# Kernel tuning notes

Hardware: AMD Instinct MI355X
Metric: run time of the kernel (lower is better)

## Reference

```python
import jax, jax.numpy as jnp
import numpy as np
import math

H = 5       # attention heads
DK = 20     # attdim // H
ATT = 100   # attdim
LAYERS = 2
B, L, BERT_DIM = 32, 256, 768


def _layernorm(x, a, b, eps=1e-6):
    mean = x.mean(-1, keepdims=True)
    std = jnp.std(x, axis=-1, ddof=1, keepdims=True)  # torch.std is unbiased
    return a * (x - mean) / (std + eps) + b


def _forward(sequence_output, src_mask, aspect_mask, short_mask,
             ln_a, ln_b, Wxx_w, Wxx_b, q_w, q_b, k_w, k_b,
             dense_w, dense_b, bias_m, W_w, W_b, Wx_w, Wx_b, clf_w, clf_b):
    Bn, Ln, _ = sequence_output.shape
    x = _layernorm(sequence_output, ln_a, ln_b)
    g = x @ Wxx_w + Wxx_b                                  # [B,L,100]
    asp_wn = aspect_mask.sum(1, keepdims=True)             # [B,1]
    aspect = (g * aspect_mask[..., None]).sum(1) / asp_wn  # [B,100]

    q = (g @ q_w + q_b).reshape(Bn, Ln, H, DK).transpose(0, 2, 1, 3)  # [B,H,L,dk]
    k = (g @ k_w + k_b).reshape(Bn, Ln, H, DK).transpose(0, 2, 1, 3)
    # aspect is expanded identically across heads/positions before dense -> [B,dk]
    asp = aspect @ dense_w + dense_b                       # [B,dk]
    scores = jnp.einsum('bhid,bhjd->bhij', q, k) / math.sqrt(DK)
    asp_sc = jnp.tanh(jnp.einsum('bd,bhjd->bhj', asp, k) + bias_m[0])
    scores = scores + asp_sc[:, :, None, :]
    scores = jnp.where(src_mask[:, None, None, :] == 0, -1e9, scores)
    scores = scores + short_mask                           # [B,1,L,L] broadcast
    adj = jax.nn.softmax(scores, axis=-1)                  # [B,H,L,L]

    # edge-update linear split so the [B,L,L,205] concat is never materialized:
    # edge[b,i,j] = adj_perm[b,i,j] @ Wa + go[b,j] @ W1 + go[b,i] @ W2 + b
    Wa, W1, W2 = Wx_w[:H], Wx_w[H:H + ATT], Wx_w[H + ATT:]
    go = g
    for i in range(LAYERS):
        # expand+matmul+mean over heads == mean-head message passing
        Ax = jnp.einsum('bhij,bjd->bid', adj, go) / H
        go = jax.nn.relu(Ax @ W_w + W_b)
        if i < LAYERS - 1:  # last edge update is discarded by the original output
            edge = (jnp.einsum('bhij,hk->bijk', adj, Wa)
                    + (go @ W1)[:, None, :, :]
                    + (go @ W2)[:, :, None, :]
                    + Wx_b)
            adj = edge.transpose(0, 3, 1, 2)
    # original: node_outputs = F.relu(gcn_outputs) (aggregate_W result is overwritten)
    h = jax.nn.relu(go)
    out1 = (h * aspect_mask[..., None]).sum(1) / asp_wn    # [B,100]
    return out1 @ clf_w + clf_b                            # [B,3]


def setup_inputs() -> dict:
    key = jax.random.key(0)
    ks = jax.random.split(key, 24)
    f32 = jnp.float32
    p = lambda k, shape, s=0.05: jax.random.normal(k, shape, dtype=f32) * s
    src_mask = jax.random.randint(ks[0], (B, L), 0, 2, dtype=jnp.int32).at[:, 0].set(1)
    aspect_mask = jnp.zeros((B, L), f32).at[:, 4:8].set(1.0)  # aspect span tokens
    return {
        'sequence_output': jax.random.normal(ks[1], (B, L, BERT_DIM), dtype=f32),
        'src_mask': src_mask,
        'aspect_mask': aspect_mask,
        'short_mask': p(ks[2], (B, 1, L, L), 1.0),
        'ln_a': jnp.ones((BERT_DIM,), f32),
        'ln_b': jnp.zeros((BERT_DIM,), f32),
        'Wxx_w': p(ks[3], (BERT_DIM, ATT)), 'Wxx_b': p(ks[4], (ATT,)),
        'q_w': p(ks[5], (ATT, ATT)), 'q_b': p(ks[6], (ATT,)),
        'k_w': p(ks[7], (ATT, ATT)), 'k_b': p(ks[8], (ATT,)),
        'dense_w': p(ks[9], (ATT, DK)), 'dense_b': p(ks[10], (DK,)),
        'bias_m': p(ks[11], (1,)),
        'W_w': p(ks[12], (ATT, ATT)), 'W_b': p(ks[13], (ATT,)),
        'Wx_w': p(ks[14], (H + 2 * ATT, H)), 'Wx_b': p(ks[15], (H,)),
        'clf_w': p(ks[16], (ATT, 3)), 'clf_b': p(ks[17], (3,)),
    }


def reference(sequence_output, src_mask, aspect_mask, short_mask,
              ln_a, ln_b, Wxx_w, Wxx_b, q_w, q_b, k_w, k_b,
              dense_w, dense_b, bias_m, W_w, W_b, Wx_w, Wx_b, clf_w, clf_b):
    return _forward(sequence_output, src_mask, aspect_mask, short_mask,
                    ln_a, ln_b, Wxx_w, Wxx_b, q_w, q_b, k_w, k_b,
                    dense_w, dense_b, bias_m, W_w, W_b, Wx_w, Wx_b, clf_w, clf_b)
```

## Files before the change

### kernel.cpp

```cpp
#include <hip/hip_runtime.h>
#include <math.h>

constexpr int CL = 256;
constexpr int CD = 768;
constexpr int CATT = 100;
constexpr int CH = 5;
constexpr int CDK = 20;

__device__ __forceinline__ void fma4(float4& a, float s, const float4& w) {
    a.x = fmaf(s, w.x, a.x);
    a.y = fmaf(s, w.y, a.y);
    a.z = fmaf(s, w.z, a.z);
    a.w = fmaf(s, w.w, a.w);
}

__device__ __forceinline__ void gl2lds16(const void* gsrc, void* ldst) {
    __builtin_amdgcn_global_load_lds(
        (const __attribute__((address_space(1))) void*)gsrc,
        (__attribute__((address_space(3))) void*)ldst, 16, 0, 0);
}

__global__ __launch_bounds__(256, 3) void k1_fused(
    const float* __restrict__ x, const float* __restrict__ ln_a,
    const float* __restrict__ ln_b, const float* __restrict__ Wxx_w,
    const float* __restrict__ Wxx_b, const float* __restrict__ q_w,
    const float* __restrict__ q_b, const float* __restrict__ k_w,
    const float* __restrict__ k_b, const float* __restrict__ amask,
    float* __restrict__ g, float* __restrict__ qt, float* __restrict__ ktb,
    float* __restrict__ aspect_raw)
{
    __shared__ float s_w[2][3200];
    __shared__ float s_xn[2][16 * 36];
    __shared__ float s_gt[16 * 100];
    __shared__ float s_ln[1536];
// ... 150 lines not shown
                float4 rv[2] = { p0, p1 };
#pragma unroll
                for (int q = 0; q < 2; ++q) {
                    int row = r0 + rg * 2 + q;
                    int bidx = row >> 8, l = row & 255;
                    *(float4*)&outp[((size_t)(bidx * CH + h) * CL + l) * CDK + d] = rv[q];
                }
                p0 = make_float4(0.f, 0.f, 0.f, 0.f);
                p1 = make_float4(0.f, 0.f, 0.f, 0.f);
            }
        }
        __syncthreads();
    }
}

__global__ __launch_bounds__(256, 3) void k45_attn_gcn0(
    const float* __restrict__ qt, const float* __restrict__ ktb,
    const float* __restrict__ aspect_raw, const float* __restrict__ amask,
    const float* __restrict__ dense_w, const float* __restrict__ dense_b,
    const float* __restrict__ bias_m, const int* __restrict__ src_mask,
    const float* __restrict__ shortm, const float* __restrict__ Wx_w,
    const float* __restrict__ g, const float* __restrict__ W_w,
    const float* __restrict__ W_b, float* __restrict__ adjW,
    float* __restrict__ go1, float* __restrict__ t1, float* __restrict__ t2,
    float* __restrict__ gW2S)
{
    constexpr int ICH = 16;
    __shared__ float s_pool[16 * 260];
    __shared__ float s_w[2][3200];
    __shared__ float s_q[CH * 320];
    __shared__ float s_red[CH][64];
    __shared__ float s_was[5];
    __shared__ float s_aspb[20];
    __shared__ float s_w1[100], s_w2[100];
    __shared__ float s_g1row[16];

    const int b = blockIdx.x >> 4, ic = blockIdx.x & 15;
    const int i0 = ic * ICH;
    const int t = threadIdx.x, lane = t & 63, wid = t >> 6;
    const int j = t;

    if (t < 5) {
        float s = 0.f;
        for (int k2 = 0; k2 < 5; ++k2) s += Wx_w[t * 5 + k2];
        s_was[t] = s;
    }
    if (t < 100) {
        float a = 0.f, c2 = 0.f;
#pragma unroll
        for (int h = 0; h < 5; ++h) {
            a += Wx_w[(5 + t) * 5 + h];
            c2 += Wx_w[(105 + t) * 5 + h];
        }
        s_w1[t] = a; s_w2[t] = c2;
    }
    float wn = 0.f;
    if (t < 64) {
        float4 mv = ((const float4*)amask)[b * 64 + t];
        wn = mv.x + mv.y + mv.z + mv.w;
#pragma unroll
        for (int o = 32; o; o >>= 1) wn += __shfl_xor(wn, o);
    }
    if (t < 20) {
        float a = 0.f;
        for (int d = 0; d < CATT; ++d)
            a = fmaf(aspect_raw[b * CATT + d], dense_w[d * CDK + t], a);
        s_aspb[t] = a / wn + dense_b[t];
    }
    {
        const float* qbase = qt + (size_t)b * CH * CL * CDK + (size_t)i0 * CDK;
        for (int i = t; i < CH * 320; i += 256) {
            int h = i / 320, r = i % 320;
            s_q[i] = qbase[(size_t)h * CL * CDK + r];
        }
    }

    const bool masked = (src_mask[b * CL + j] == 0);
    const float bm = bias_m[0];
    const float rs20 = 0.223606797749978969f;

    float sm[ICH];
#pragma unroll
    for (int ii = 0; ii < ICH; ++ii)
        sm[ii] = shortm[(size_t)(b * CL + i0 + ii) * CL + j];

    float accS[ICH], accW[ICH];
#pragma unroll
    for (int ii = 0; ii < ICH; ++ii) { accS[ii] = 0.f; accW[ii] = 0.f; }

    __syncthreads();

    for (int h = 0; h < CH; ++h) {
        float4 kr[5];
        const float* kp = ktb + ((size_t)(b * CH + h) * CL + j) * CDK;
#pragma unroll
        for (int m = 0; m < 5; ++m) kr[m] = *(const float4*)(kp + 4 * m);
        const float was_h = s_was[h];
        float s = bm;
#pragma unroll
        for (int m = 0; m < 5; ++m) {
            s = fmaf(s_aspb[4 * m + 0], kr[m].x, s);
            s = fmaf(s_aspb[4 * m + 1], kr[m].y, s);
            s = fmaf(s_aspb[4 * m + 2], kr[m].z, s);
            s = fmaf(s_aspb[4 * m + 3], kr[m].w, s);
        }
        const float aspsc = tanhf(s);

        float pv[ICH];
#pragma unroll
        for (int ii = 0; ii < ICH; ++ii) {
            const float* qrow = &s_q[h * 320 + ii * CDK];
            float sc = 0.f;
#pragma unroll
            for (int m = 0; m < 5; ++m) {
                float4 q4 = *(const float4*)(qrow + 4 * m);
                sc = fmaf(q4.x, kr[m].x, sc);
                sc = fmaf(q4.y, kr[m].y, sc);
                sc = fmaf(q4.z, kr[m].z, sc);
                sc = fmaf(q4.w, kr[m].w, sc);
            }
            sc = fmaf(sc, rs20, aspsc) + sm[ii];
            float p = masked ? 0.f : __expf(sc);
            pv[ii] = p;
            float ssum = p;
#pragma unroll
            for (int o = 32; o; o >>= 1) ssum += __shfl_xor(ssum, o);
            if (lane == 0) s_red[h][ii * 4 + wid] = ssum;
        }
        __syncthreads();
#pragma unroll
        for (int ii = 0; ii < ICH; ++ii) {
            float tot = s_red[h][ii * 4 + 0] + s_red[h][ii * 4 + 1] +
                        s_red[h][ii * 4 + 2] + s_red[h][ii * 4 + 3];
            float pn = pv[ii] * __frcp_rn(tot);
            accS[ii] += pn;
            accW[ii] = fmaf(was_h, pn, accW[ii]);
        }
    }

#pragma unroll
    for (int ii = 0; ii < ICH; ++ii) {
        adjW[(size_t)(b * CL + i0 + ii) * CL + j] = accW[ii];
        s_pool[ii * 260 + j] = accS[ii];
    }

    const int cg = t % 25, rg = t / 25;
    const int c = cg * 4;
    const float4* g4 = (const float4*)g + (size_t)b * 6400;
    gl2lds16(g4 + t,       &s_w[0][(t      ) * 4]);
    gl2lds16(g4 + t + 256, &s_w[0][(t + 256) * 4]);
    gl2lds16(g4 + t + 512, &s_w[0][(t + 512) * 4]);
    if (t < 32) gl2lds16(g4 + t + 768, &s_w[0][(t + 768) * 4]);
    __syncthreads();

    float4 acc0 = make_float4(0.f, 0.f, 0.f, 0.f);
    float4 acc1 = make_float4(0.f, 0.f, 0.f, 0.f);
    for (int jt = 0; jt < 8; ++jt) {
        if (jt < 7) {
            const float4* src = g4 + (size_t)(jt + 1) * 800;
            float* wd = s_w[(jt + 1) & 1];
            gl2lds16(src + t,       wd + (t      ) * 4);
            gl2lds16(src + t + 256, wd + (t + 256) * 4);
            gl2lds16(src + t + 512, wd + (t + 512) * 4);
            if (t < 32) gl2lds16(src + t + 768, wd + (t + 768) * 4);
        }
        if (t < 200) {
            const float* wb = s_w[jt & 1];
#pragma unroll 2
            for (int kk = 0; kk < 32; kk += 4) {
                float4 a0 = *(const float4*)&s_pool[(rg * 2 + 0) * 260 + jt * 32 + kk];
                float4 a1 = *(const float4*)&s_pool[(rg * 2 + 1) * 260 + jt * 32 + kk];
                float4 v0 = *(const float4*)&wb[(kk + 0) * 100 + c];
                float4 v1 = *(const float4*)&wb[(kk + 1) * 100 + c];
                float4 v2 = *(const float4*)&wb[(kk + 2) * 100 + c];
                float4 v3 = *(const float4*)&wb[(kk + 3) * 100 + c];
                fma4(acc0, a0.x, v0); fma4(acc0, a0.y, v1); fma4(acc0, a0.z, v2); fma4(acc0, a0.w, v3);
                fma4(acc1, a1.x, v0); fma4(acc1, a1.y, v1); fma4(acc1, a1.z, v2); fma4(acc1, a1.w, v3);
            }
        }
        __syncthreads();
    }

    float* s_ax = s_pool;
    if (t < 200) {
        float4 r;
        r.x = acc0.x * 0.2f; r.y = acc0.y * 0.2f; r.z = acc0.z * 0.2f; r.w = acc0.w * 0.2f;
        *(float4*)&s_ax[(rg * 2 + 0) * 108 + c] = r;
        r.x = acc1.x * 0.2f; r.y = acc1.y * 0.2f; r.z = acc1.z * 0.2f; r.w = acc1.w * 0.2f;
        *(float4*)&s_ax[(rg * 2 + 1) * 108 + c] = r;
    }
    const float4* ww4 = (const float4*)W_w;
    gl2lds16(ww4 + t, &s_w[0][t * 4]);
    if (t < 244) gl2lds16(ww4 + t + 256, &s_w[0][(t + 256) * 4]);
    __syncthreads();

    float4 o0 = make_float4(0.f, 0.f, 0.f, 0.f);
    float4 o1 = make_float4(0.f, 0.f, 0.f, 0.f);
    for (int wt = 0; wt < 5; ++wt) {
        if (wt < 4) {
            const float4* src = ww4 + (size_t)(wt + 1) * 500;
            float* wd = s_w[(wt + 1) & 1];
            gl2lds16(src + t, wd + t * 4);
            if (t < 244) gl2lds16(src + t + 256, wd + (t + 256) * 4);
        }
        if (t < 200) {
            const float* wb = s_w[wt & 1];
            const int kb = wt * 20;
#pragma unroll 2
            for (int kk = 0; kk < 20; kk += 4) {
                float4 a0 = *(const float4*)&s_ax[(rg * 2 + 0) * 108 + kb + kk];
                float4 a1 = *(const float4*)&s_ax[(rg * 2 + 1) * 108 + kb + kk];
                float4 v0 = *(const float4*)&wb[(kk + 0) * 100 + c];
                float4 v1 = *(const float4*)&wb[(kk + 1) * 100 + c];
                float4 v2 = *(const float4*)&wb[(kk + 2) * 100 + c];
                float4 v3 = *(const float4*)&wb[(kk + 3) * 100 + c];
                fma4(o0, a0.x, v0); fma4(o0, a0.y, v1); fma4(o0, a0.z, v2); fma4(o0, a0.w, v3);
                fma4(o1, a1.x, v0); fma4(o1, a1.y, v1); fma4(o1, a1.z, v2); fma4(o1, a1.w, v3);
            }
        }
        __syncthreads();
    }

    float* s_go = s_pool + 1728;
    if (t < 200) {
        float4 bias = *(const float4*)&W_b[c];
        o0.x = fmaxf(o0.x + bias.x, 0.f); o0.y = fmaxf(o0.y + bias.y, 0.f);
        o0.z = fmaxf(o0.z + bias.z, 0.f); o0.w = fmaxf(o0.w + bias.w, 0.f);
        o1.x = fmaxf(o1.x + bias.x, 0.f); o1.y = fmaxf(o1.y + bias.y, 0.f);
        o1.z = fmaxf(o1.z + bias.z, 0.f); o1.w = fmaxf(o1.w + bias.w, 0.f);
        *(float4*)&go1[(size_t)(b * CL + i0 + rg * 2 + 0) * CATT + c] = o0;
        *(float4*)&go1[(size_t)(b * CL + i0 + rg * 2 + 1) * CATT + c] = o1;
        *(float4*)&s_go[(rg * 2 + 0) * 104 + c] = o0;
        *(float4*)&s_go[(rg * 2 + 1) * 104 + c] = o1;
    }
    __syncthreads();

    if (t < 128) {
        int r = t >> 3, seg = t & 7;
        int e0 = seg * 13, e1 = e0 + 13 < 100 ? e0 + 13 : 100;
        float a = 0.f, c2 = 0.f;
        for (int e = e0; e < e1; ++e) {
            float v = s_go[r * 104 + e];
            a = fmaf(v, s_w1[e], a);
            c2 = fmaf(v, s_w2[e], c2);
        }
        a += __shfl_xor(a, 1); a += __shfl_xor(a, 2); a += __shfl_xor(a, 4);
        c2 += __shfl_xor(c2, 1); c2 += __shfl_xor(c2, 2); c2 += __shfl_xor(c2, 4);
        if (seg == 0) {
            s_g1row[r] = a;
            gW2S[b * CL + i0 + r] = c2;
        }
    }
    __syncthreads();

    if (t < 100) {
        float a = 0.f, s2 = 0.f;
#pragma unroll
        for (int r = 0; r < 16; ++r) {
            float v = s_go[r * 104 + t];
            a = fmaf(s_g1row[r], v, a);
            s2 += v;
        }
        atomicAdd(&t1[b * CATT + t], a);
        atomicAdd(&t2[b * CATT + t], s2);
    }
}

__global__ __launch_bounds__(256, 3) void k7_gcn1(
    const float* __restrict__ adjW, const float* __restrict__ go1,
    const float* __restrict__ W_w, const float* __restrict__ W_b,
    const float* __restrict__ t1, const float* __restrict__ t2,
    const float* __restrict__ gW2S, const float* __restrict__ Wx_b,
    const float* __restrict__ amask, float* __restrict__ out1_raw)
{
    __shared__ float s_pool[16 * 260];
    __shared__ float s_w[2][3200];
    const int b = blockIdx.x >> 4, ic = blockIdx.x & 15;
    const int i0 = ic * 16;
    const int t = threadIdx.x;

    {
        const float4* asrc = (const float4*)adjW + (size_t)(b * CL + i0) * 64;
#pragma unroll
        for (int m = 0; m < 4; ++m) {
            int i = t + 256 * m;
            gl2lds16(asrc + i, &s_pool[(i >> 6) * 260 + (i & 63) * 4]);
        }
    }
    const int cg = t % 25, rg = t / 25;
    const int c = cg * 4;
    const float4* g4 = (const float4*)go1 + (size_t)b * 6400;
    gl2lds16(g4 + t,       &s_w[0][(t      ) * 4]);
    gl2lds16(g4 + t + 256, &s_w[0][(t + 256) * 4]);
    gl2lds16(g4 + t + 512, &s_w[0][(t + 512) * 4]);
    if (t < 32) gl2lds16(g4 + t + 768, &s_w[0][(t + 768) * 4]);
    __syncthreads();

    float4 acc0 = make_float4(0.f, 0.f, 0.f, 0.f);
    float4 acc1 = make_float4(0.f, 0.f, 0.f, 0.f);
    for (int jt = 0; jt < 8; ++jt) {
        if (jt < 7) {
            const float4* src = g4 + (size_t)(jt + 1) * 800;
            float* wd = s_w[(jt + 1) & 1];
            gl2lds16(src + t,       wd + (t      ) * 4);
            gl2lds16(src + t + 256, wd + (t + 256) * 4);
            gl2lds16(src + t + 512, wd + (t + 512) * 4);
            if (t < 32) gl2lds16(src + t + 768, wd + (t + 768) * 4);
        }
        if (t < 200) {
            const float* wb = s_w[jt & 1];
#pragma unroll 2
            for (int kk = 0; kk < 32; kk += 4) {
                float4 a0 = *(const float4*)&s_pool[(rg * 2 + 0) * 260 + jt * 32 + kk];
                float4 a1 = *(const float4*)&s_pool[(rg * 2 + 1) * 260 + jt * 32 + kk];
                float4 v0 = *(const float4*)&wb[(kk + 0) * 100 + c];
                float4 v1 = *(const float4*)&wb[(kk + 1) * 100 + c];
                float4 v2 = *(const float4*)&wb[(kk + 2) * 100 + c];
                float4 v3 = *(const float4*)&wb[(kk + 3) * 100 + c];
                fma4(acc0, a0.x, v0); fma4(acc0, a0.y, v1); fma4(acc0, a0.z, v2); fma4(acc0, a0.w, v3);
                fma4(acc1, a1.x, v0); fma4(acc1, a1.y, v1); fma4(acc1, a1.z, v2); fma4(acc1, a1.w, v3);
            }
        }
        __syncthreads();
    }

    float* s_ax = s_pool;
    if (t < 200) {
        float wxbs = Wx_b[0] + Wx_b[1] + Wx_b[2] + Wx_b[3] + Wx_b[4];
        float4 t1v = *(const float4*)&t1[b * CATT + c];
        float4 t2v = *(const float4*)&t2[b * CATT + c];
        float gw0 = gW2S[b * CL + i0 + rg * 2 + 0] + wxbs;
        float gw1 = gW2S[b * CL + i0 + rg * 2 + 1] + wxbs;
        float4 r;
        r.x = (acc0.x + t1v.x + gw0 * t2v.x) * 0.2f;
        r.y = (acc0.y + t1v.y + gw0 * t2v.y) * 0.2f;
        r.z = (acc0.z + t1v.z + gw0 * t2v.z) * 0.2f;
        r.w = (acc0.w + t1v.w + gw0 * t2v.w) * 0.2f;
        *(float4*)&s_ax[(rg * 2 + 0) * 108 + c] = r;
        r.x = (acc1.x + t1v.x + gw1 * t2v.x) * 0.2f;
        r.y = (acc1.y + t1v.y + gw1 * t2v.y) * 0.2f;
        r.z = (acc1.z + t1v.z + gw1 * t2v.z) * 0.2f;
        r.w = (acc1.w + t1v.w + gw1 * t2v.w) * 0.2f;
        *(float4*)&s_ax[(rg * 2 + 1) * 108 + c] = r;
    }
    const float4* ww4 = (const float4*)W_w;
    gl2lds16(ww4 + t, &s_w[0][t * 4]);
    if (t < 244) gl2lds16(ww4 + t + 256, &s_w[0][(t + 256) * 4]);
    __syncthreads();

    float4 o0 = make_float4(0.f, 0.f, 0.f, 0.f);
    float4 o1 = make_float4(0.f, 0.f, 0.f, 0.f);
    for (int wt = 0; wt < 5; ++wt) {
        if (wt < 4) {
            const float4* src = ww4 + (size_t)(wt + 1) * 500;
            float* wd = s_w[(wt + 1) & 1];
            gl2lds16(src + t, wd + t * 4);
            if (t < 244) gl2lds16(src + t + 256, wd + (t + 256) * 4);
        }
        if (t < 200) {
            const float* wb = s_w[wt & 1];
            const int kb = wt * 20;
#pragma unroll 2
            for (int kk = 0; kk < 20; kk += 4) {
                float4 a0 = *(const float4*)&s_ax[(rg * 2 + 0) * 108 + kb + kk];
                float4 a1 = *(const float4*)&s_ax[(rg * 2 + 1) * 108 + kb + kk];
                float4 v0 = *(const float4*)&wb[(kk + 0) * 100 + c];
                float4 v1 = *(const float4*)&wb[(kk + 1) * 100 + c];
                float4 v2 = *(const float4*)&wb[(kk + 2) * 100 + c];
                float4 v3 = *(const float4*)&wb[(kk + 3) * 100 + c];
                fma4(o0, a0.x, v0); fma4(o0, a0.y, v1); fma4(o0, a0.z, v2); fma4(o0, a0.w, v3);
                fma4(o1, a1.x, v0); fma4(o1, a1.y, v1); fma4(o1, a1.z, v2); fma4(o1, a1.w, v3);
            }
        }
        __syncthreads();
    }

    if (t < 200) {
        float4 bias = *(const float4*)&W_b[c];
        o0.x = fmaxf(o0.x + bias.x, 0.f); o0.y = fmaxf(o0.y + bias.y, 0.f);
        o0.z = fmaxf(o0.z + bias.z, 0.f); o0.w = fmaxf(o0.w + bias.w, 0.f);
        o1.x = fmaxf(o1.x + bias.x, 0.f); o1.y = fmaxf(o1.y + bias.y, 0.f);
        o1.z = fmaxf(o1.z + bias.z, 0.f); o1.w = fmaxf(o1.w + bias.w, 0.f);
        float4 ov[2] = { o0, o1 };
#pragma unroll
        for (int q = 0; q < 2; ++q) {
            int row = b * CL + i0 + rg * 2 + q;
            float m = amask[row];
            if (m != 0.f) {
                atomicAdd(&out1_raw[b * CATT + c + 0], m * ov[q].x);
                atomicAdd(&out1_raw[b * CATT + c + 1], m * ov[q].y);
                atomicAdd(&out1_raw[b * CATT + c + 2], m * ov[q].z);
                atomicAdd(&out1_raw[b * CATT + c + 3], m * ov[q].w);
            }
        }
    }
}

__global__ __launch_bounds__(64) void k8_small(
    const float* __restrict__ out1_raw, const float* __restrict__ amask,
    const float* __restrict__ clf_w, const float* __restrict__ clf_b,
    float* __restrict__ out)
{
    const int b = blockIdx.x, t = threadIdx.x;
    float4 mv = ((const float4*)amask)[b * 64 + t];
    float wn = mv.x + mv.y + mv.z + mv.w;
#pragma unroll
    for (int o = 32; o; o >>= 1) wn += __shfl_xor(wn, o);
    if (t < 3) {
        float rwn = 1.f / wn;
        float a = clf_b[t];
        for (int d = 0; d < CATT; ++d)
            a = fmaf(out1_raw[b * CATT + d] * rwn, clf_w[d * 3 + t], a);
        out[b * 3 + t] = a;
    }
}

extern "C" void kernel_launch(void* const* d_in, const int* in_sizes, int n_in,
                              void* d_out, int out_size, void* d_ws, size_t ws_size,
                              hipStream_t stream) {
    const float* seq     = (const float*)d_in[0];
    const int*   srcm    = (const int*)d_in[1];
    const float* amask   = (const float*)d_in[2];
    const float* shortm  = (const float*)d_in[3];
    const float* ln_a    = (const float*)d_in[4];
    const float* ln_b    = (const float*)d_in[5];
    const float* Wxx_w   = (const float*)d_in[6];
    const float* Wxx_b   = (const float*)d_in[7];
    const float* q_w     = (const float*)d_in[8];
// ... 4 lines not shown
    const float* dense_b = (const float*)d_in[13];
    const float* bias_m  = (const float*)d_in[14];
    const float* W_w     = (const float*)d_in[15];
    const float* W_b     = (const float*)d_in[16];
    const float* Wx_w    = (const float*)d_in[17];
    const float* Wx_b    = (const float*)d_in[18];
    const float* clf_w   = (const float*)d_in[19];
    const float* clf_b   = (const float*)d_in[20];
    float* out = (float*)d_out;

    float* ws         = (float*)d_ws;
    float* g          = ws;
    float* qt         = g + 819200;
    float* ktb        = qt + 819200;
    float* go1        = ktb + 819200;
    float* adjW       = go1 + 819200;
    float* aspect_raw = adjW + 2097152;
    float* t1         = aspect_raw + 3200;
    float* t2         = t1 + 3200;
    float* out1_raw   = t2 + 3200;
    float* gW2S       = out1_raw + 3200;

    hipMemsetAsync(aspect_raw, 0, 4 * 3200 * sizeof(float), stream);
    hipLaunchKernelGGL(k1_fused, dim3(512), dim3(256), 0, stream, seq, ln_a, ln_b,
                       Wxx_w, Wxx_b, q_w, q_b, k_w, k_b, amask, g, qt, ktb, aspect_raw);
    hipLaunchKernelGGL(k45_attn_gcn0, dim3(512), dim3(256), 0, stream,
                       qt, ktb, aspect_raw, amask, dense_w, dense_b, bias_m, srcm,
                       shortm, Wx_w, g, W_w, W_b, adjW, go1, t1, t2, gW2S);
    hipLaunchKernelGGL(k7_gcn1, dim3(512), dim3(256), 0, stream,
                       adjW, go1, W_w, W_b, t1, t2, gW2S, Wx_b, amask, out1_raw);
    hipLaunchKernelGGL(k8_small, dim3(32), dim3(64), 0, stream,
                       out1_raw, amask, clf_w, clf_b, out);
}
```

Baseline: 241.3 us.

## Fuse attention, both GCN layers and classifier into one kernel with per-batch barriers

Merges the attention/GCN0 kernel, the GCN1 kernel and the classifier kernel into one launch. Blocks that share a batch synchronise through per-batch atomic counters in global memory, and the block grid is remapped so that a batch's blocks land on the same XCD. The adjW matrix stays in registers instead of being written to and re-read from global memory, which removes two launches and a large intermediate. The cost is spin-wait barriers that depend on all 16 blocks of a batch being co-resident, which risks deadlock or stalls if occupancy is insufficient.

```diff
diff --git a/kernel.cpp b/kernel.cpp
--- a/kernel.cpp
+++ b/kernel.cpp
@@ -18,6 +18,20 @@
     __builtin_amdgcn_global_load_lds(
         (const __attribute__((address_space(1))) void*)gsrc,
         (__attribute__((address_space(3))) void*)ldst, 16, 0, 0);
+}
+
+__device__ __forceinline__ void bbar(unsigned* ctr, unsigned target, bool poll) {
+    __syncthreads();
+    if (threadIdx.x == 0) {
+        __hip_atomic_fetch_add(ctr, 1u, __ATOMIC_RELEASE, __HIP_MEMORY_SCOPE_AGENT);
+        if (poll) {
+            while (__hip_atomic_load(ctr, __ATOMIC_RELAXED, __HIP_MEMORY_SCOPE_AGENT) < target) {
+                __builtin_amdgcn_s_sleep(2);
+            }
+        }
+    }
+    __syncthreads();
+    __builtin_amdgcn_fence(__ATOMIC_ACQUIRE, "agent");
 }
 
 __global__ __launch_bounds__(256, 3) void k1_fused(
@@ -198,16 +212,18 @@
     }
 }
 
-__global__ __launch_bounds__(256, 3) void k45_attn_gcn0(
+__global__ __launch_bounds__(256, 3) void k457_fused(
     const float* __restrict__ qt, const float* __restrict__ ktb,
     const float* __restrict__ aspect_raw, const float* __restrict__ amask,
     const float* __restrict__ dense_w, const float* __restrict__ dense_b,
     const float* __restrict__ bias_m, const int* __restrict__ src_mask,
     const float* __restrict__ shortm, const float* __restrict__ Wx_w,
     const float* __restrict__ g, const float* __restrict__ W_w,
-    const float* __restrict__ W_b, float* __restrict__ adjW,
+    const float* __restrict__ W_b, const float* __restrict__ Wx_b,
+    const float* __restrict__ clf_w, const float* __restrict__ clf_b,
     float* __restrict__ go1, float* __restrict__ t1, float* __restrict__ t2,
-    float* __restrict__ gW2S)
+    float* __restrict__ out1_raw, unsigned* __restrict__ bar,
+    float* __restrict__ out)
 {
     constexpr int ICH = 16;
     __shared__ float s_pool[16 * 260];
@@ -218,384 +234,375 @@
     __shared__ float s_aspb[20];
     __shared__ float s_w1[100], s_w2[100];
     __shared__ float s_g1row[16];
-
-    const int b = blockIdx.x >> 4, ic = blockIdx.x & 15;
+    __shared__ float s_gw2[16];
+
+    const int t = threadIdx.x, lane = t & 63, wid = t >> 6;
+    const int xcd = blockIdx.x & 7;
+    const int slot = blockIdx.x >> 3;
+    const int b = xcd * 4 + (slot >> 4);
+    const int ic = slot & 15;
     const int i0 = ic * ICH;
-    const int t = threadIdx.x, lane = t & 63, wid = t >> 6;
     const int j = t;
-
-    if (t < 5) {
-        float s = 0.f;
-        for (int k2 = 0; k2 < 5; ++k2) s += Wx_w[t * 5 + k2];
-        s_was[t] = s;
-    }
-    if (t < 100) {
-        float a = 0.f, c2 = 0.f;
-#pragma unroll
-        for (int h = 0; h < 5; ++h) {
-            a += Wx_w[(5 + t) * 5 + h];
-            c2 += Wx_w[(105 + t) * 5 + h];
-        }
-        s_w1[t] = a; s_w2[t] = c2;
-    }
-    float wn = 0.f;
-    if (t < 64) {
-        float4 mv = ((const float4*)amask)[b * 64 + t];
-        wn = mv.x + mv.y + mv.z + mv.w;
-#pragma unroll
-        for (int o = 32; o; o >>= 1) wn += __shfl_xor(wn, o);
-    }
-    if (t < 20) {
-        float a = 0.f;
-        for (int d = 0; d < CATT; ++d)
-            a = fmaf(aspect_raw[b * CATT + d], dense_w[d * CDK + t], a);
-        s_aspb[t] = a / wn + dense_b[t];
-    }
+    unsigned* bctr = bar + b * 32;
+
+    float accW[ICH];
     {
-        const float* qbase = qt + (size_t)b * CH * CL * CDK + (size_t)i0 * CDK;
-        for (int i = t; i < CH * 320; i += 256) {
-            int h = i / 320, r = i % 320;
-            s_q[i] = qbase[(size_t)h * CL * CDK + r];
-        }
-    }
-
-    const bool masked = (src_mask[b * CL + j] == 0);
-    const float bm = bias_m[0];
-    const float rs20 = 0.223606797749978969f;
-
-    float sm[ICH];
-#pragma unroll
-    for (int ii = 0; ii < ICH; ++ii)
-        sm[ii] = shortm[(size_t)(b * CL + i0 + ii) * CL + j];
-
-    float accS[ICH], accW[ICH];
-#pragma unroll
-    for (int ii = 0; ii < ICH; ++ii) { accS[ii] = 0.f; accW[ii] = 0.f; }
-
-    __syncthreads();
-
-    for (int h = 0; h < CH; ++h) {
-        float4 kr[5];
-        const float* kp = ktb + ((size_t)(b * CH + h) * CL + j) * CDK;
-#pragma unroll
-        for (int m = 0; m < 5; ++m) kr[m] = *(const float4*)(kp + 4 * m);
-        const float was_h = s_was[h];
-        float s = bm;
-#pragma unroll
-        for (int m = 0; m < 5; ++m) {
-            s = fmaf(s_aspb[4 * m + 0], kr[m].x, s);
-            s = fmaf(s_aspb[4 * m + 1], kr[m].y, s);
-            s = fmaf(s_aspb[4 * m + 2], kr[m].z, s);
-            s = fmaf(s_aspb[4 * m + 3], kr[m].w, s);
-        }
-        const float aspsc = tanhf(s);
-
-        float pv[ICH];
-#pragma unroll
-        for (int ii = 0; ii < ICH; ++ii) {
-            const float* qrow = &s_q[h * 320 + ii * CDK];
-            float sc = 0.f;
+        if (t < 5) {
+            float s = 0.f;
+            for (int k2 = 0; k2 < 5; ++k2) s += Wx_w[t * 5 + k2];
+            s_was[t] = s;
+        }
+        if (t < 100) {
+            float a = 0.f, c2 = 0.f;
+#pragma unroll
+            for (int h = 0; h < 5; ++h) {
+                a += Wx_w[(5 + t) * 5 + h];
+                c2 += Wx_w[(105 + t) * 5 + h];
+            }
+            s_w1[t] = a; s_w2[t] = c2;
+        }
+        float wn = 0.f;
+        if (t < 64) {
+            float4 mv = ((const float4*)amask)[b * 64 + t];
+            wn = mv.x + mv.y + mv.z + mv.w;
+#pragma unroll
+            for (int o = 32; o; o >>= 1) wn += __shfl_xor(wn, o);
+        }
+        if (t < 20) {
+            float a = 0.f;
+            for (int d = 0; d < CATT; ++d)
+                a = fmaf(aspect_raw[b * CATT + d], dense_w[d * CDK + t], a);
+            s_aspb[t] = a / wn + dense_b[t];
+        }
+        {
+            const float* qbase = qt + (size_t)b * CH * CL * CDK + (size_t)i0 * CDK;
+            for (int i = t; i < CH * 320; i += 256) {
+                int h = i / 320, r = i % 320;
+                s_q[i] = qbase[(size_t)h * CL * CDK + r];
+            }
+        }
+
+        const bool masked = (src_mask[b * CL + j] == 0);
+        const float bm = bias_m[0];
+        const float rs20 = 0.223606797749978969f;
+
+        float sm[ICH];
+#pragma unroll
+        for (int ii = 0; ii < ICH; ++ii)
+            sm[ii] = shortm[(size_t)(b * CL + i0 + ii) * CL + j];
+
+        float accS[ICH];
+#pragma unroll
+        for (int ii = 0; ii < ICH; ++ii) { accS[ii] = 0.f; accW[ii] = 0.f; }
+
+        __syncthreads();
+
+        for (int h = 0; h < CH; ++h) {
+            float4 kr[5];
+            const float* kp = ktb + ((size_t)(b * CH + h) * CL + j) * CDK;
+#pragma unroll
+            for (int m = 0; m < 5; ++m) kr[m] = *(const float4*)(kp + 4 * m);
+            const float was_h = s_was[h];
+            float s = bm;
 #pragma unroll
             for (int m = 0; m < 5; ++m) {
-                float4 q4 = *(const float4*)(qrow + 4 * m);
-                sc = fmaf(q4.x, kr[m].x, sc);
-                sc = fmaf(q4.y, kr[m].y, sc);
-                sc = fmaf(q4.z, kr[m].z, sc);
-                sc = fmaf(q4.w, kr[m].w, sc);
-            }
-            sc = fmaf(sc, rs20, aspsc) + sm[ii];
-            float p = masked ? 0.f : __expf(sc);
-            pv[ii] = p;
-            float ssum = p;
-#pragma unroll
-            for (int o = 32; o; o >>= 1) ssum += __shfl_xor(ssum, o);
-            if (lane == 0) s_red[h][ii * 4 + wid] = ssum;
-        }
-        __syncthreads();
-#pragma unroll
-        for (int ii = 0; ii < ICH; ++ii) {
-            float tot = s_red[h][ii * 4 + 0] + s_red[h][ii * 4 + 1] +
-                        s_red[h][ii * 4 + 2] + s_red[h][ii * 4 + 3];
-            float pn = pv[ii] * __frcp_rn(tot);
-            accS[ii] += pn;
-            accW[ii] = fmaf(was_h, pn, accW[ii]);
-        }
-    }
-
-#pragma unroll
-    for (int ii = 0; ii < ICH; ++ii) {
-        adjW[(size_t)(b * CL + i0 + ii) * CL + j] = accW[ii];
-        s_pool[ii * 260 + j] = accS[ii];
+                s = fmaf(s_aspb[4 * m + 0], kr[m].x, s);
+                s = fmaf(s_aspb[4 * m + 1], kr[m].y, s);
+                s = fmaf(s_aspb[4 * m + 2], kr[m].z, s);
+                s = fmaf(s_aspb[4 * m + 3], kr[m].w, s);
+            }
+            const float aspsc = tanhf(s);
+
+            float pv[ICH];
+#pragma unroll
+            for (int ii = 0; ii < ICH; ++ii) {
+                const float* qrow = &s_q[h * 320 + ii * CDK];
+                float sc = 0.f;
+#pragma unroll
+                for (int m = 0; m < 5; ++m) {
+                    float4 q4 = *(const float4*)(qrow + 4 * m);
+                    sc = fmaf(q4.x, kr[m].x, sc);
+                    sc = fmaf(q4.y, kr[m].y, sc);
+                    sc = fmaf(q4.z, kr[m].z, sc);
+                    sc = fmaf(q4.w, kr[m].w, sc);
+                }
+                sc = fmaf(sc, rs20, aspsc) + sm[ii];
+                float p = masked ? 0.f : __expf(sc);
+                pv[ii] = p;
+                float ssum = p;
+#pragma unroll
+                for (int o = 32; o; o >>= 1) ssum += __shfl_xor(ssum, o);
+                if (lane == 0) s_red[h][ii * 4 + wid] = ssum;
+            }
+            __syncthreads();
+#pragma unroll
+            for (int ii = 0; ii < ICH; ++ii) {
+                float tot = s_red[h][ii * 4 + 0] + s_red[h][ii * 4 + 1] +
+                            s_red[h][ii * 4 + 2] + s_red[h][ii * 4 + 3];
+                float pn = pv[ii] * __frcp_rn(tot);
+                accS[ii] += pn;
+                accW[ii] = fmaf(was_h, pn, accW[ii]);
+            }
+        }
+
+#pragma unroll
+        for (int ii = 0; ii < ICH; ++ii)
+            s_pool[ii * 260 + j] = accS[ii];
     }
 
     const int cg = t % 25, rg = t / 25;
     const int c = cg * 4;
-    const float4* g4 = (const float4*)g + (size_t)b * 6400;
-    gl2lds16(g4 + t,       &s_w[0][(t      ) * 4]);
-    gl2lds16(g4 + t + 256, &s_w[0][(t + 256) * 4]);
-    gl2lds16(g4 + t + 512, &s_w[0][(t + 512) * 4]);
-    if (t < 32) gl2lds16(g4 + t + 768, &s_w[0][(t + 768) * 4]);
-    __syncthreads();
-
-    float4 acc0 = make_float4(0.f, 0.f, 0.f, 0.f);
-    float4 acc1 = make_float4(0.f, 0.f, 0.f, 0.f);
-    for (int jt = 0; jt < 8; ++jt) {
-        if (jt < 7) {
-            const float4* src = g4 + (size_t)(jt + 1) * 800;
-            float* wd = s_w[(jt + 1) & 1];
-            gl2lds16(src + t,       wd + (t      ) * 4);
-            gl2lds16(src + t + 256, wd + (t + 256) * 4);
-            gl2lds16(src + t + 512, wd + (t + 512) * 4);
-            if (t < 32) gl2lds16(src + t + 768, wd + (t + 768) * 4);
-        }
+
+    {
+        const float4* g4 = (const float4*)g + (size_t)b * 6400;
+        gl2lds16(g4 + t,       &s_w[0][(t      ) * 4]);
+        gl2lds16(g4 + t + 256, &s_w[0][(t + 256) * 4]);
+        gl2lds16(g4 + t + 512, &s_w[0][(t + 512) * 4]);
+        if (t < 32) gl2lds16(g4 + t + 768, &s_w[0][(t + 768) * 4]);
+        __syncthreads();
+
+        float4 acc0 = make_float4(0.f, 0.f, 0.f, 0.f);
+        float4 acc1 = make_float4(0.f, 0.f, 0.f, 0.f);
+        for (int jt = 0; jt < 8; ++jt) {
+            if (jt < 7) {
+                const float4* src = g4 + (size_t)(jt + 1) * 800;
+                float* wd = s_w[(jt + 1) & 1];
+                gl2lds16(src + t,       wd + (t      ) * 4);
+                gl2lds16(src + t + 256, wd + (t + 256) * 4);
+                gl2lds16(src + t + 512, wd + (t + 512) * 4);
+                if (t < 32) gl2lds16(src + t + 768, wd + (t + 768) * 4);
+            }
+            if (t < 200) {
+                const float* wb = s_w[jt & 1];
+#pragma unroll 2
+                for (int kk = 0; kk < 32; kk += 4) {
+                    float4 a0 = *(const float4*)&s_pool[(rg * 2 + 0) * 260 + jt * 32 + kk];
+                    float4 a1 = *(const float4*)&s_pool[(rg * 2 + 1) * 260 + jt * 32 + kk];
+                    float4 v0 = *(const float4*)&wb[(kk + 0) * 100 + c];
+                    float4 v1 = *(const float4*)&wb[(kk + 1) * 100 + c];
+                    float4 v2 = *(const float4*)&wb[(kk + 2) * 100 + c];
+                    float4 v3 = *(const float4*)&wb[(kk + 3) * 100 + c];
+                    fma4(acc0, a0.x, v0); fma4(acc0, a0.y, v1); fma4(acc0, a0.z, v2); fma4(acc0, a0.w, v3);
+                    fma4(acc1, a1.x, v0); fma4(acc1, a1.y, v1); fma4(acc1, a1.z, v2); fma4(acc1, a1.w, v3);
+                }
+            }
+            __syncthreads();
+        }
+
+        float* s_ax = s_pool;
         if (t < 200) {
-            const float* wb = s_w[jt & 1];
+            float4 r;
+            r.x = acc0.x * 0.2f; r.y = acc0.y * 0.2f; r.z = acc0.z * 0.2f; r.w = acc0.w * 0.2f;
+            *(float4*)&s_ax[(rg * 2 + 0) * 108 + c] = r;
+            r.x = acc1.x * 0.2f; r.y = acc1.y * 0.2f; r.z = acc1.z * 0.2f; r.w = acc1.w * 0.2f;
+            *(float4*)&s_ax[(rg * 2 + 1) * 108 + c] = r;
+        }
+        const float4* ww4 = (const float4*)W_w;
+        gl2lds16(ww4 + t, &s_w[0][t * 4]);
+        if (t < 244) gl2lds16(ww4 + t + 256, &s_w[0][(t + 256) * 4]);
+        __syncthreads();
+
+        float4 o0 = make_float4(0.f, 0.f, 0.f, 0.f);
+        float4 o1 = make_float4(0.f, 0.f, 0.f, 0.f);
+        for (int wt = 0; wt < 5; ++wt) {
+            if (wt < 4) {
+                const float4* src = ww4 + (size_t)(wt + 1) * 500;
+                float* wd = s_w[(wt + 1) & 1];
+                gl2lds16(src + t, wd + t * 4);
+                if (t < 244) gl2lds16(src + t + 256, wd + (t + 256) * 4);
+            }
+            if (t < 200) {
+                const float* wb = s_w[wt & 1];
+                const int kb = wt * 20;
 #pragma unroll 2
-            for (int kk = 0; kk < 32; kk += 4) {
-                float4 a0 = *(const float4*)&s_pool[(rg * 2 + 0) * 260 + jt * 32 + kk];
-                float4 a1 = *(const float4*)&s_pool[(rg * 2 + 1) * 260 + jt * 32 + kk];
-                float4 v0 = *(const float4*)&wb[(kk + 0) * 100 + c];
-                float4 v1 = *(const float4*)&wb[(kk + 1) * 100 + c];
-                float4 v2 = *(const float4*)&wb[(kk + 2) * 100 + c];
-                float4 v3 = *(const float4*)&wb[(kk + 3) * 100 + c];
-                fma4(acc0, a0.x, v0); fma4(acc0, a0.y, v1); fma4(acc0, a0.z, v2); fma4(acc0, a0.w, v3);
-                fma4(acc1, a1.x, v0); fma4(acc1, a1.y, v1); fma4(acc1, a1.z, v2); fma4(acc1, a1.w, v3);
-            }
-        }
-        __syncthreads();
-    }
-
-    float* s_ax = s_pool;
-    if (t < 200) {
-        float4 r;
-        r.x = acc0.x * 0.2f; r.y = acc0.y * 0.2f; r.z = acc0.z * 0.2f; r.w = acc0.w * 0.2f;
-        *(float4*)&s_ax[(rg * 2 + 0) * 108 + c] = r;
-        r.x = acc1.x * 0.2f; r.y = acc1.y * 0.2f; r.z = acc1.z * 0.2f; r.w = acc1.w * 0.2f;
-        *(float4*)&s_ax[(rg * 2 + 1) * 108 + c] = r;
-    }
-    const float4* ww4 = (const float4*)W_w;
-    gl2lds16(ww4 + t, &s_w[0][t * 4]);
-    if (t < 244) gl2lds16(ww4 + t + 256, &s_w[0][(t + 256) * 4]);
-    __syncthreads();
-
-    float4 o0 = make_float4(0.f, 0.f, 0.f, 0.f);
-    float4 o1 = make_float4(0.f, 0.f, 0.f, 0.f);
-    for (int wt = 0; wt < 5; ++wt) {
-        if (wt < 4) {
-            const float4* src = ww4 + (size_t)(wt + 1) * 500;
-            float* wd = s_w[(wt + 1) & 1];
-            gl2lds16(src + t, wd + t * 4);
-            if (t < 244) gl2lds16(src + t + 256, wd + (t + 256) * 4);
-        }
+                for (int kk = 0; kk < 20; kk += 4) {
+                    float4 a0 = *(const float4*)&s_ax[(rg * 2 + 0) * 108 + kb + kk];
+                    float4 a1 = *(const float4*)&s_ax[(rg * 2 + 1) * 108 + kb + kk];
+                    float4 v0 = *(const float4*)&wb[(kk + 0) * 100 + c];
+                    float4 v1 = *(const float4*)&wb[(kk + 1) * 100 + c];
+                    float4 v2 = *(const float4*)&wb[(kk + 2) * 100 + c];
+                    float4 v3 = *(const float4*)&wb[(kk + 3) * 100 + c];
+                    fma4(o0, a0.x, v0); fma4(o0, a0.y, v1); fma4(o0, a0.z, v2); fma4(o0, a0.w, v3);
+                    fma4(o1, a1.x, v0); fma4(o1, a1.y, v1); fma4(o1, a1.z, v2); fma4(o1, a1.w, v3);
+                }
+            }
+            __syncthreads();
+        }
+
+        float* s_go = s_pool + 1728;
         if (t < 200) {
-            const float* wb = s_w[wt & 1];
-            const int kb = wt * 20;
+            float4 bias = *(const float4*)&W_b[c];
+            o0.x = fmaxf(o0.x + bias.x, 0.f); o0.y = fmaxf(o0.y + bias.y, 0.f);
+            o0.z = fmaxf(o0.z + bias.z, 0.f); o0.w = fmaxf(o0.w + bias.w, 0.f);
+            o1.x = fmaxf(o1.x + bias.x, 0.f); o1.y = fmaxf(o1.y + bias.y, 0.f);
+            o1.z = fmaxf(o1.z + bias.z, 0.f); o1.w = fmaxf(o1.w + bias.w, 0.f);
+            *(float4*)&go1[(size_t)(b * CL + i0 + rg * 2 + 0) * CATT + c] = o0;
+            *(float4*)&go1[(size_t)(b * CL + i0 + rg * 2 + 1) * CATT + c] = o1;
+            *(float4*)&s_go[(rg * 2 + 0) * 104 + c] = o0;
+            *(float4*)&s_go[(rg * 2 + 1) * 104 + c] = o1;
+        }
+        __syncthreads();
+
+        if (t < 128) {
+            int r = t >> 3, seg = t & 7;
+            int e0 = seg * 13, e1 = e0 + 13 < 100 ? e0 + 13 : 100;
+            float a = 0.f, c2 = 0.f;
+            for (int e = e0; e < e1; ++e) {
+                float v = s_go[r * 104 + e];
+                a = fmaf(v, s_w1[e], a);
+                c2 = fmaf(v, s_w2[e], c2);
+            }
+            a += __shfl_xor(a, 1); a += __shfl_xor(a, 2); a += __shfl_xor(a, 4);
+            c2 += __shfl_xor(c2, 1); c2 += __shfl_xor(c2, 2); c2 += __shfl_xor(c2, 4);
+            if (seg == 0) {
+                s_g1row[r] = a;
+                s_gw2[r] = c2;
+            }
+        }
+        __syncthreads();
+
+        if (t < 100) {
+            float a = 0.f, s2 = 0.f;
+#pragma unroll
+            for (int r = 0; r < 16; ++r) {
+                float v = s_go[r * 104 + t];
+                a = fmaf(s_g1row[r], v, a);
+                s2 += v;
+            }
+            atomicAdd(&t1[b * CATT + t], a);
+            atomicAdd(&t2[b * CATT + t], s2);
+        }
+        __syncthreads();
+
+#pragma unroll
+        for (int ii = 0; ii < ICH; ++ii)
+            s_pool[ii * 260 + j] = accW[ii];
+    }
+
+    bbar(bctr, 16, true);
+
+    {
+        const float4* g4 = (const float4*)go1 + (size_t)b * 6400;
+        gl2lds16(g4 + t,       &s_w[0][(t      ) * 4]);
+        gl2lds16(g4 + t + 256, &s_w[0][(t + 256) * 4]);
+        gl2lds16(g4 + t + 512, &s_w[0][(t + 512) * 4]);
+        if (t < 32) gl2lds16(g4 + t + 768, &s_w[0][(t + 768) * 4]);
+        __syncthreads();
+
+        float4 acc0 = make_float4(0.f, 0.f, 0.f, 0.f);
+        float4 acc1 = make_float4(0.f, 0.f, 0.f, 0.f);
+        for (int jt = 0; jt < 8; ++jt) {
+            if (jt < 7) {
+                const float4* src = g4 + (size_t)(jt + 1) * 800;
+                float* wd = s_w[(jt + 1) & 1];
+                gl2lds16(src + t,       wd + (t      ) * 4);
+                gl2lds16(src + t + 256, wd + (t + 256) * 4);
+                gl2lds16(src + t + 512, wd + (t + 512) * 4);
+                if (t < 32) gl2lds16(src + t + 768, wd + (t + 768) * 4);
+            }
+            if (t < 200) {
+                const float* wb = s_w[jt & 1];
 #pragma unroll 2
-            for (int kk = 0; kk < 20; kk += 4) {
-                float4 a0 = *(const float4*)&s_ax[(rg * 2 + 0) * 108 + kb + kk];
-                float4 a1 = *(const float4*)&s_ax[(rg * 2 + 1) * 108 + kb + kk];
-                float4 v0 = *(const float4*)&wb[(kk + 0) * 100 + c];
-                float4 v1 = *(const float4*)&wb[(kk + 1) * 100 + c];
-                float4 v2 = *(const float4*)&wb[(kk + 2) * 100 + c];
-                float4 v3 = *(const float4*)&wb[(kk + 3) * 100 + c];
-                fma4(o0, a0.x, v0); fma4(o0, a0.y, v1); fma4(o0, a0.z, v2); fma4(o0, a0.w, v3);
-                fma4(o1, a1.x, v0); fma4(o1, a1.y, v1); fma4(o1, a1.z, v2); fma4(o1, a1.w, v3);
-            }
-        }
-        __syncthreads();
-    }
-
-    float* s_go = s_pool + 1728;
-    if (t < 200) {
-        float4 bias = *(const float4*)&W_b[c];
-        o0.x = fmaxf(o0.x + bias.x, 0.f); o0.y = fmaxf(o0.y + bias.y, 0.f);
-        o0.z = fmaxf(o0.z + bias.z, 0.f); o0.w = fmaxf(o0.w + bias.w, 0.f);
-        o1.x = fmaxf(o1.x + bias.x, 0.f); o1.y = fmaxf(o1.y + bias.y, 0.f);
-        o1.z = fmaxf(o1.z + bias.z, 0.f); o1.w = fmaxf(o1.w + bias.w, 0.f);
-        *(float4*)&go1[(size_t)(b * CL + i0 + rg * 2 + 0) * CATT + c] = o0;
-        *(float4*)&go1[(size_t)(b * CL + i0 + rg * 2 + 1) * CATT + c] = o1;
-        *(float4*)&s_go[(rg * 2 + 0) * 104 + c] = o0;
-        *(float4*)&s_go[(rg * 2 + 1) * 104 + c] = o1;
-    }
-    __syncthreads();
-
-    if (t < 128) {
-        int r = t >> 3, seg = t & 7;
-        int e0 = seg * 13, e1 = e0 + 13 < 100 ? e0 + 13 : 100;
-        float a = 0.f, c2 = 0.f;
-        for (int e = e0; e < e1; ++e) {
-            float v = s_go[r * 104 + e];
-            a = fmaf(v, s_w1[e], a);
-            c2 = fmaf(v, s_w2[e], c2);
-        }
-        a += __shfl_xor(a, 1); a += __shfl_xor(a, 2); a += __shfl_xor(a, 4);
-        c2 += __shfl_xor(c2, 1); c2 += __shfl_xor(c2, 2); c2 += __shfl_xor(c2, 4);
-        if (seg == 0) {
-            s_g1row[r] = a;
-            gW2S[b * CL + i0 + r] = c2;
-        }
-    }
-    __syncthreads();
-
-    if (t < 100) {
-        float a = 0.f, s2 = 0.f;
-#pragma unroll
-        for (int r = 0; r < 16; ++r) {
-            float v = s_go[r * 104 + t];
-            a = fmaf(s_g1row[r], v, a);
-            s2 += v;
-        }
-        atomicAdd(&t1[b * CATT + t], a);
-        atomicAdd(&t2[b * CATT + t], s2);
-    }
-}
-
-__global__ __launch_bounds__(256, 3) void k7_gcn1(
-    const float* __restrict__ adjW, const float* __restrict__ go1,
-    const float* __restrict__ W_w, const float* __restrict__ W_b,
-    const float* __restrict__ t1, const float* __restrict__ t2,
-    const float* __restrict__ gW2S, const float* __restrict__ Wx_b,
-    const float* __restrict__ amask, float* __restrict__ out1_raw)
-{
-    __shared__ float s_pool[16 * 260];
-    __shared__ float s_w[2][3200];
-    const int b = blockIdx.x >> 4, ic = blockIdx.x & 15;
-    const int i0 = ic * 16;
-    const int t = threadIdx.x;
-
-    {
-        const float4* asrc = (const float4*)adjW + (size_t)(b * CL + i0) * 64;
-#pragma unroll
-        for (int m = 0; m < 4; ++m) {
-            int i = t + 256 * m;
-            gl2lds16(asrc + i, &s_pool[(i >> 6) * 260 + (i & 63) * 4]);
-        }
-    }
-    const int cg = t % 25, rg = t / 25;
-    const int c = cg * 4;
-    const float4* g4 = (const float4*)go1 + (size_t)b * 6400;
-    gl2lds16(g4 + t,       &s_w[0][(t      ) * 4]);
-    gl2lds16(g4 + t + 256, &s_w[0][(t + 256) * 4]);
-    gl2lds16(g4 + t + 512, &s_w[0][(t + 512) * 4]);
-    if (t < 32) gl2lds16(g4 + t + 768, &s_w[0][(t + 768) * 4]);
-    __syncthreads();
-
-    float4 acc0 = make_float4(0.f, 0.f, 0.f, 0.f);
-    float4 acc1 = make_float4(0.f, 0.f, 0.f, 0.f);
-    for (int jt = 0; jt < 8; ++jt) {
-        if (jt < 7) {
-            const float4* src = g4 + (size_t)(jt + 1) * 800;
-            float* wd = s_w[(jt + 1) & 1];
-            gl2lds16(src + t,       wd + (t      ) * 4);
-            gl2lds16(src + t + 256, wd + (t + 256) * 4);
-            gl2lds16(src + t + 512, wd + (t + 512) * 4);
-            if (t < 32) gl2lds16(src + t + 768, wd + (t + 768) * 4);
-        }
+                for (int kk = 0; kk < 32; kk += 4) {
+                    float4 a0 = *(const float4*)&s_pool[(rg * 2 + 0) * 260 + jt * 32 + kk];
+                    float4 a1 = *(const float4*)&s_pool[(rg * 2 + 1) * 260 + jt * 32 + kk];
+                    float4 v0 = *(const float4*)&wb[(kk + 0) * 100 + c];
+                    float4 v1 = *(const float4*)&wb[(kk + 1) * 100 + c];
+                    float4 v2 = *(const float4*)&wb[(kk + 2) * 100 + c];
+                    float4 v3 = *(const float4*)&wb[(kk + 3) * 100 + c];
+                    fma4(acc0, a0.x, v0); fma4(acc0, a0.y, v1); fma4(acc0, a0.z, v2); fma4(acc0, a0.w, v3);
+                    fma4(acc1, a1.x, v0); fma4(acc1, a1.y, v1); fma4(acc1, a1.z, v2); fma4(acc1, a1.w, v3);
+                }
+            }
+            __syncthreads();
+        }
+
+        float* s_ax = s_pool;
         if (t < 200) {
-            const float* wb = s_w[jt & 1];
+            float wxbs = Wx_b[0] + Wx_b[1] + Wx_b[2] + Wx_b[3] + Wx_b[4];
+            float4 t1v = *(const float4*)&t1[b * CATT + c];
+            float4 t2v = *(const float4*)&t2[b * CATT + c];
+            float gw0 = s_gw2[rg * 2 + 0] + wxbs;
+            float gw1 = s_gw2[rg * 2 + 1] + wxbs;
+            float4 r;
+            r.x = (acc0.x + t1v.x + gw0 * t2v.x) * 0.2f;
+            r.y = (acc0.y + t1v.y + gw0 * t2v.y) * 0.2f;
+            r.z = (acc0.z + t1v.z + gw0 * t2v.z) * 0.2f;
+            r.w = (acc0.w + t1v.w + gw0 * t2v.w) * 0.2f;
+            *(float4*)&s_ax[(rg * 2 + 0) * 108 + c] = r;
+            r.x = (acc1.x + t1v.x + gw1 * t2v.x) * 0.2f;
+            r.y = (acc1.y + t1v.y + gw1 * t2v.y) * 0.2f;
+            r.z = (acc1.z + t1v.z + gw1 * t2v.z) * 0.2f;
+            r.w = (acc1.w + t1v.w + gw1 * t2v.w) * 0.2f;
+            *(float4*)&s_ax[(rg * 2 + 1) * 108 + c] = r;
+        }
+        const float4* ww4 = (const float4*)W_w;
+        gl2lds16(ww4 + t, &s_w[0][t * 4]);
+        if (t < 244) gl2lds16(ww4 + t + 256, &s_w[0][(t + 256) * 4]);
+        __syncthreads();
+
+        float4 o0 = make_float4(0.f, 0.f, 0.f, 0.f);
+        float4 o1 = make_float4(0.f, 0.f, 0.f, 0.f);
+        for (int wt = 0; wt < 5; ++wt) {
+            if (wt < 4) {
+                const float4* src = ww4 + (size_t)(wt + 1) * 500;
+                float* wd = s_w[(wt + 1) & 1];
+                gl2lds16(src + t, wd + t * 4);
+                if (t < 244) gl2lds16(src + t + 256, wd + (t + 256) * 4);
+            }
+            if (t < 200) {
+                const float* wb = s_w[wt & 1];
+                const int kb = wt * 20;
 #pragma unroll 2
-            for (int kk = 0; kk < 32; kk += 4) {
-                float4 a0 = *(const float4*)&s_pool[(rg * 2 + 0) * 260 + jt * 32 + kk];
-                float4 a1 = *(const float4*)&s_pool[(rg * 2 + 1) * 260 + jt * 32 + kk];
-                float4 v0 = *(const float4*)&wb[(kk + 0) * 100 + c];
-                float4 v1 = *(const float4*)&wb[(kk + 1) * 100 + c];
-                float4 v2 = *(const float4*)&wb[(kk + 2) * 100 + c];
-                float4 v3 = *(const float4*)&wb[(kk + 3) * 100 + c];
-                fma4(acc0, a0.x, v0); fma4(acc0, a0.y, v1); fma4(acc0, a0.z, v2); fma4(acc0, a0.w, v3);
-                fma4(acc1, a1.x, v0); fma4(acc1, a1.y, v1); fma4(acc1, a1.z, v2); fma4(acc1, a1.w, v3);
-            }
-        }
-        __syncthreads();
-    }
-
-    float* s_ax = s_pool;
-    if (t < 200) {
-        float wxbs = Wx_b[0] + Wx_b[1] + Wx_b[2] + Wx_b[3] + Wx_b[4];
-        float4 t1v = *(const float4*)&t1[b * CATT + c];
-        float4 t2v = *(const float4*)&t2[b * CATT + c];
-        float gw0 = gW2S[b * CL + i0 + rg * 2 + 0] + wxbs;
-        float gw1 = gW2S[b * CL + i0 + rg * 2 + 1] + wxbs;
-        float4 r;
-        r.x = (acc0.x + t1v.x + gw0 * t2v.x) * 0.2f;
-        r.y = (acc0.y + t1v.y + gw0 * t2v.y) * 0.2f;
-        r.z = (acc0.z + t1v.z + gw0 * t2v.z) * 0.2f;
-        r.w = (acc0.w + t1v.w + gw0 * t2v.w) * 0.2f;
-        *(float4*)&s_ax[(rg * 2 + 0) * 108 + c] = r;
-        r.x = (acc1.x + t1v.x + gw1 * t2v.x) * 0.2f;
-        r.y = (acc1.y + t1v.y + gw1 * t2v.y) * 0.2f;
-        r.z = (acc1.z + t1v.z + gw1 * t2v.z) * 0.2f;
-        r.w = (acc1.w + t1v.w + gw1 * t2v.w) * 0.2f;
-        *(float4*)&s_ax[(rg * 2 + 1) * 108 + c] = r;
-    }
-    const float4* ww4 = (const float4*)W_w;
-    gl2lds16(ww4 + t, &s_w[0][t * 4]);
-    if (t < 244) gl2lds16(ww4 + t + 256, &s_w[0][(t + 256) * 4]);
-    __syncthreads();
-
-    float4 o0 = make_float4(0.f, 0.f, 0.f, 0.f);
-    float4 o1 = make_float4(0.f, 0.f, 0.f, 0.f);
-    for (int wt = 0; wt < 5; ++wt) {
-        if (wt < 4) {
-            const float4* src = ww4 + (size_t)(wt + 1) * 500;
-            float* wd = s_w[(wt + 1) & 1];
-            gl2lds16(src + t, wd + t * 4);
-            if (t < 244) gl2lds16(src + t + 256, wd + (t + 256) * 4);
-        }
+                for (int kk = 0; kk < 20; kk += 4) {
+                    float4 a0 = *(const float4*)&s_ax[(rg * 2 + 0) * 108 + kb + kk];
+                    float4 a1 = *(const float4*)&s_ax[(rg * 2 + 1) * 108 + kb + kk];
+                    float4 v0 = *(const float4*)&wb[(kk + 0) * 100 + c];
+                    float4 v1 = *(const float4*)&wb[(kk + 1) * 100 + c];
+                    float4 v2 = *(const float4*)&wb[(kk + 2) * 100 + c];
+                    float4 v3 = *(const float4*)&wb[(kk + 3) * 100 + c];
+                    fma4(o0, a0.x, v0); fma4(o0, a0.y, v1); fma4(o0, a0.z, v2); fma4(o0, a0.w, v3);
+                    fma4(o1, a1.x, v0); fma4(o1, a1.y, v1); fma4(o1, a1.z, v2); fma4(o1, a1.w, v3);
+                }
+            }
+            __syncthreads();
+        }
+
         if (t < 200) {
-            const float* wb = s_w[wt & 1];
-            const int kb = wt * 20;
-#pragma unroll 2
-            for (int kk = 0; kk < 20; kk += 4) {
-                float4 a0 = *(const float4*)&s_ax[(rg * 2 + 0) * 108 + kb + kk];
-                float4 a1 = *(const float4*)&s_ax[(rg * 2 + 1) * 108 + kb + kk];
-                float4 v0 = *(const float4*)&wb[(kk + 0) * 100 + c];
-                float4 v1 = *(const float4*)&wb[(kk + 1) * 100 + c];
-                float4 v2 = *(const float4*)&wb[(kk + 2) * 100 + c];
-                float4 v3 = *(const float4*)&wb[(kk + 3) * 100 + c];
-                fma4(o0, a0.x, v0); fma4(o0, a0.y, v1); fma4(o0, a0.z, v2); fma4(o0, a0.w, v3);
-                fma4(o1, a1.x, v0); fma4(o1, a1.y, v1); fma4(o1, a1.z, v2); fma4(o1, a1.w, v3);
-            }
-        }
-        __syncthreads();
-    }
-
-    if (t < 200) {
-        float4 bias = *(const float4*)&W_b[c];
-        o0.x = fmaxf(o0.x + bias.x, 0.f); o0.y = fmaxf(o0.y + bias.y, 0.f);
-        o0.z = fmaxf(o0.z + bias.z, 0.f); o0.w = fmaxf(o0.w + bias.w, 0.f);
-        o1.x = fmaxf(o1.x + bias.x, 0.f); o1.y = fmaxf(o1.y + bias.y, 0.f);
-        o1.z = fmaxf(o1.z + bias.z, 0.f); o1.w = fmaxf(o1.w + bias.w, 0.f);
-        float4 ov[2] = { o0, o1 };
-#pragma unroll
-        for (int q = 0; q < 2; ++q) {
-            int row = b * CL + i0 + rg * 2 + q;
-            float m = amask[row];
-            if (m != 0.f) {
-                atomicAdd(&out1_raw[b * CATT + c + 0], m * ov[q].x);
-                atomicAdd(&out1_raw[b * CATT + c + 1], m * ov[q].y);
-                atomicAdd(&out1_raw[b * CATT + c + 2], m * ov[q].z);
-                atomicAdd(&out1_raw[b * CATT + c + 3], m * ov[q].w);
-            }
-        }
-    }
-}
-
-__global__ __launch_bounds__(64) void k8_small(
-    const float* __restrict__ out1_raw, const float* __restrict__ amask,
-    const float* __restrict__ clf_w, const float* __restrict__ clf_b,
-    float* __restrict__ out)
-{
-    const int b = blockIdx.x, t = threadIdx.x;
-    float4 mv = ((const float4*)amask)[b * 64 + t];
-    float wn = mv.x + mv.y + mv.z + mv.w;
-#pragma unroll
-    for (int o = 32; o; o >>= 1) wn += __shfl_xor(wn, o);
-    if (t < 3) {
-        float rwn = 1.f / wn;
-        float a = clf_b[t];
-        for (int d = 0; d < CATT; ++d)
-            a = fmaf(out1_raw[b * CATT + d] * rwn, clf_w[d * 3 + t], a);
-        out[b * 3 + t] = a;
+            float4 bias = *(const float4*)&W_b[c];
+            o0.x = fmaxf(o0.x + bias.x, 0.f); o0.y = fmaxf(o0.y + bias.y, 0.f);
+            o0.z = fmaxf(o0.z + bias.z, 0.f); o0.w = fmaxf(o0.w + bias.w, 0.f);
+            o1.x = fmaxf(o1.x + bias.x, 0.f); o1.y = fmaxf(o1.y + bias.y, 0.f);
+            o1.z = fmaxf(o1.z + bias.z, 0.f); o1.w = fmaxf(o1.w + bias.w, 0.f);
+            float4 ov[2] = { o0, o1 };
+#pragma unroll
+            for (int q = 0; q < 2; ++q) {
+                int row = b * CL + i0 + rg * 2 + q;
+                float m = amask[row];
+                if (m != 0.f) {
+                    atomicAdd(&out1_raw[b * CATT + c + 0], m * ov[q].x);
+                    atomicAdd(&out1_raw[b * CATT + c + 1], m * ov[q].y);
+                    atomicAdd(&out1_raw[b * CATT + c + 2], m * ov[q].z);
+                    atomicAdd(&out1_raw[b * CATT + c + 3], m * ov[q].w);
+                }
+            }
+        }
+    }
+
+    bbar(bctr, 32, ic == 0);
+
+    if (ic == 0 && t < 64) {
+        float4 mv = ((const float4*)amask)[b * 64 + t];
+        float wn = mv.x + mv.y + mv.z + mv.w;
+#pragma unroll
+        for (int o = 32; o; o >>= 1) wn += __shfl_xor(wn, o);
+        if (t < 3) {
+            float rwn = 1.f / wn;
+            float a = clf_b[t];
+            for (int d = 0; d < CATT; ++d)
+                a = fmaf(out1_raw[b * CATT + d] * rwn, clf_w[d * 3 + t], a);
+            out[b * 3 + t] = a;
+        }
     }
 }
 
@@ -630,21 +637,18 @@
     float* qt         = g + 819200;
     float* ktb        = qt + 819200;
     float* go1        = ktb + 819200;
-    float* adjW       = go1 + 819200;
-    float* aspect_raw = adjW + 2097152;
+    float* aspect_raw = go1 + 819200;
     float* t1         = aspect_raw + 3200;
     float* t2         = t1 + 3200;
     float* out1_raw   = t2 + 3200;
-    float* gW2S       = out1_raw + 3200;
-
-    hipMemsetAsync(aspect_raw, 0, 4 * 3200 * sizeof(float), stream);
+    unsigned* bar     = (unsigned*)(out1_raw + 3200);
+
+    hipMemsetAsync(aspect_raw, 0,
+                   4 * 3200 * sizeof(float) + 32 * 32 * sizeof(unsigned), stream);
     hipLaunchKernelGGL(k1_fused, dim3(512), dim3(256), 0, stream, seq, ln_a, ln_b,
                        Wxx_w, Wxx_b, q_w, q_b, k_w, k_b, amask, g, qt, ktb, aspect_raw);
-    hipLaunchKernelGGL(k45_attn_gcn0, dim3(512), dim3(256), 0, stream,
+    hipLaunchKernelGGL(k457_fused, dim3(512), dim3(256), 0, stream,
                        qt, ktb, aspect_raw, amask, dense_w, dense_b, bias_m, srcm,
-                       shortm, Wx_w, g, W_w, W_b, adjW, go1, t1, t2, gW2S);
-    hipLaunchKernelGGL(k7_gcn1, dim3(512), dim3(256), 0, stream,
-                       adjW, go1, W_w, W_b, t1, t2, gW2S, Wx_b, amask, out1_raw);
-    hipLaunchKernelGGL(k8_small, dim3(32), dim3(64), 0, stream,
-                       out1_raw, amask, clf_w, clf_b, out);
+                       shortm, Wx_w, g, W_w, W_b, Wx_b, clf_w, clf_b,
+                       go1, t1, t2, out1_raw, bar, out);
 }
```

After: 267.4 us. 1.11x slower.
